# Performance work log

Hardware: AMD Instinct MI355X
Metric: run time of the kernel (lower is better)

## Reference

```python
import jax, jax.numpy as jnp
import numpy as np

B, N, F, P = 8, 16384, 128, 28


def setup_inputs() -> dict:
    key = jax.random.key(0)
    k1, k2 = jax.random.split(key)
    x = jax.random.uniform(k1, (B, N, 2), dtype=jnp.float32)  # 2D coords in [0,1]
    sigma = jnp.full((1,), np.log(0.05), dtype=jnp.float32)   # learned log-lengthscale
    image_features = jax.random.normal(k2, (F, P, P), dtype=jnp.float32) / np.sqrt(F)
    return {"x": x, "sigma": sigma, "image_features": image_features}


def reference(x, sigma, image_features):
    # x: [B, N, 2], sigma: [1] (log lengthscale), image_features: [F, P, P]
    P_ = image_features.shape[-1]
    grid = jnp.linspace(0.001, 1.0 - 0.001, P_, dtype=x.dtype)  # [P]
    ls = jnp.exp(sigma[0])                                      # lengthscale
    inv = 0.5 / (ls * ls)
    # pairwise squared dists grid vs each coordinate axis -> [B, P, N]
    d0 = (grid[None, :, None] - x[:, None, :, 0]) ** 2
    d1 = (grid[None, :, None] - x[:, None, :, 1]) ** 2
    k0 = jnp.exp(-inv * d0)  # [B, P, N]
    k1 = jnp.exp(-inv * d1)  # [B, P, N]
    # features[b,n,f] = sum_{p,q} k0[b,p,n] * IF[f,p,q] * k1[b,q,n]
    feats = jnp.einsum('bpn,fpq,bqn->bnf', k0, image_features, k1)
    return feats
```

## Files before the change

kernel.cpp:

```cpp
#include <hip/hip_runtime.h>
#include <stdint.h>

#define BDIM   8
#define NDIM   16384
#define FDIM   128
#define PDIM   28
#define MPTS   (BDIM * NDIM)
#define SLICE  4096
#define HSLICE 2048
#define TPTS   256
#define TILES  2
#define CPTS   (TPTS * TILES)

typedef _Float16 half8  __attribute__((ext_vector_type(8)));
typedef _Float16 half4  __attribute__((ext_vector_type(4)));
typedef float    floatx4 __attribute__((ext_vector_type(4)));

__global__ __launch_bounds__(256) void prep_ift(const float* __restrict__ IF,
                                                _Float16* __restrict__ IFt) {
    int idx = blockIdx.x * 256 + threadIdx.x;
    int kk  = idx >> 12;
    int rem = idx & 4095;
    int f   = rem >> 5;
    int s   = (rem >> 3) & 3;
    int j   = idx & 7;
    int q   = ((s ^ ((f >> 1) & 3)) << 3) + j;
    float v = (q < PDIM) ? IF[f * (PDIM * PDIM) + kk * PDIM + q] : 0.0f;
    IFt[idx] = (_Float16)v;
}

__device__ __forceinline__ void gload16(const _Float16* g, _Float16* l) {
    __builtin_amdgcn_global_load_lds(
        (const __attribute__((address_space(1))) void*)g,
        (__attribute__((address_space(3))) void*)l, 16, 0, 0);
}

__global__ __launch_bounds__(512, 1) void feats_kernel(
    const float* __restrict__ x,
    const float* __restrict__ sigma,
    const _Float16* __restrict__ IFt,
    float* __restrict__ out)
{
    __shared__ __align__(16) _Float16 bs [PDIM * HSLICE];
    __shared__ __align__(16) _Float16 k1s[TPTS * 40];
    __shared__ __align__(16) _Float16 k0t[PDIM * TPTS];

    const int tid   = threadIdx.x;
    const int lane  = tid & 63;
    const int wave  = tid >> 6;
    const int wm    = wave >> 1;
    const int wn    = wave & 1;
    const int ln15  = lane & 15;
    const int quad  = lane >> 4;
    const int chunk = blockIdx.x >> 1;
    const int h     = blockIdx.x & 1;

    if (tid < 256) {
        const _Float16* g = IFt + h * HSLICE + tid * 8;
        #pragma unroll
        for (int kk = 0; kk < PDIM; kk++)
            gload16(g + kk * SLICE, &bs[kk * HSLICE + tid * 8]);
    }

    const float ls    = __expf(sigma[0]);
    const float inv   = 0.5f / (ls * ls);
    const float gstep = 0.998f / 27.0f;

    int bfo[2];
    #pragma unroll
    for (int nt = 0; nt < 2; nt++) {
        const int fl = wn * 32 + nt * 16 + ln15;
        bfo[nt] = fl * 32 + ((quad ^ ((fl >> 1) & 3)) << 3);
    }
    const int k0o  = wm * 64 + ln15 * 4;
    const int k1ro = wm * 64 + ln15;

    #pragma unroll 1
    for (int tile = 0; tile < TILES; tile++) {
        {
            const int ptl = tid & 255;
            const int ptg = chunk * CPTS + tile * TPTS + ptl;
            if (tid < 256) {
                const float x0 = x[2 * ptg + 0];
                const int base = (ptl >> 6) * 64 + (ptl & 15) * 4 + ((ptl >> 4) & 3);
                #pragma unroll
                for (int p = 0; p < PDIM; p++) {
                    float d = (0.001f + p * gstep) - x0;
                    k0t[p * TPTS + base] = (_Float16)__expf(-inv * d * d);
                }
            } else {
                const float x1 = x[2 * ptg + 1];
                #pragma unroll
                for (int q = 0; q < PDIM; q++) {
                    float d = (0.001f + q * gstep) - x1;
                    k1s[ptl * 40 + q] = (_Float16)__expf(-inv * d * d);
                }
                #pragma unroll
                for (int q = PDIM; q < 32; q++)
                    k1s[ptl * 40 + q] = (_Float16)0.0f;
            }
        }
        __syncthreads();

        half8 k1f[4];
        #pragma unroll
        for (int mt = 0; mt < 4; mt++)
            k1f[mt] = *(const half8*)&k1s[(k1ro + mt * 16) * 40 + quad * 8];

        floatx4 acc[4][2];
        #pragma unroll
        for (int mt = 0; mt < 4; mt++)
            #pragma unroll
            for (int nt = 0; nt < 2; nt++)
                acc[mt][nt] = (floatx4){0.0f, 0.0f, 0.0f, 0.0f};

        #pragma unroll 4
        for (int kk = 0; kk < PDIM; kk++) {
            half8 bf[2];
            #pragma unroll
            for (int nt = 0; nt < 2; nt++)
                bf[nt] = *(const half8*)&bs[kk * HSLICE + bfo[nt]];
            const half4 k0v = *(const half4*)&k0t[kk * TPTS + k0o];
            #pragma unroll
            for (int mt = 0; mt < 4; mt++) {
                const half8 af = k1f[mt] * k0v[mt];
                #pragma unroll
                for (int nt = 0; nt < 2; nt++)
                    acc[mt][nt] = __builtin_amdgcn_mfma_f32_16x16x32_f16(
                        af, bf[nt], acc[mt][nt], 0, 0, 0);
            }
        }

        #pragma unroll
        for (int mt = 0; mt < 4; mt++) {
            const int row0 = chunk * CPTS + tile * TPTS + wm * 64 + mt * 16 + quad * 4;
            #pragma unroll
            for (int nt = 0; nt < 2; nt++) {
                const int col = h * 64 + wn * 32 + nt * 16 + ln15;
                float* op = out + (size_t)row0 * FDIM + col;
                #pragma unroll
                for (int r = 0; r < 4; r++)
                    __builtin_nontemporal_store(acc[mt][nt][r], op + (size_t)r * FDIM);
            }
        }

        if (tile + 1 < TILES)
            __syncthreads();
    }
}

extern "C" void kernel_launch(void* const* d_in, const int* in_sizes, int n_in,
                              void* d_out, int out_size, void* d_ws, size_t ws_size,
                              hipStream_t stream) {
    const float* x     = (const float*)d_in[0];
    const float* sigma = (const float*)d_in[1];
    const float* IF    = (const float*)d_in[2];
    float* out = (float*)d_out;

    _Float16* IFt = (_Float16*)d_ws;

    prep_ift<<<(PDIM * SLICE) / 256, 256, 0, stream>>>(IF, IFt);
    feats_kernel<<<(MPTS / CPTS) * 2, 512, 0, stream>>>(x, sigma, IFt, out);
}
```

Before: 101.7 us.

## Split features into quarters, double-buffer k0 tiles, compute k1 in registers

Each block now handles a quarter of the feature dimension (32 columns) over four 256-point tiles, which shrinks the LDS footprint so launch bounds can allow four blocks per CU. The k0 Gaussian table is double-buffered and the next tile is filled while the current one is computed, leaving a single barrier per tile. k1 fragments are computed straight into registers per wave instead of being staged through LDS. The trade-off is that k0/k1 exponentials are recomputed across four times as many blocks and there are fewer MFMAs per wave per tile.

```diff
diff --git a/kernel.cpp b/kernel.cpp
--- a/kernel.cpp
+++ b/kernel.cpp
@@ -7,13 +7,13 @@
 #define PDIM   28
 #define MPTS   (BDIM * NDIM)
 #define SLICE  4096
-#define HSLICE 2048
+#define QSL    1024
 #define TPTS   256
-#define TILES  2
+#define TILES  4
 #define CPTS   (TPTS * TILES)
 
 typedef _Float16 half8  __attribute__((ext_vector_type(8)));
-typedef _Float16 half4  __attribute__((ext_vector_type(4)));
+typedef _Float16 half2v __attribute__((ext_vector_type(2)));
 typedef float    floatx4 __attribute__((ext_vector_type(4)));
 
 __global__ __launch_bounds__(256) void prep_ift(const float* __restrict__ IF,
@@ -35,94 +35,97 @@
         (__attribute__((address_space(3))) void*)l, 16, 0, 0);
 }
 
-__global__ __launch_bounds__(512, 1) void feats_kernel(
+__global__ __launch_bounds__(512, 4) void feats_kernel(
     const float* __restrict__ x,
     const float* __restrict__ sigma,
     const _Float16* __restrict__ IFt,
     float* __restrict__ out)
 {
-    __shared__ __align__(16) _Float16 bs [PDIM * HSLICE];
-    __shared__ __align__(16) _Float16 k1s[TPTS * 40];
-    __shared__ __align__(16) _Float16 k0t[PDIM * TPTS];
+    __shared__ __align__(16) _Float16 bs [PDIM * QSL];
+    __shared__ __align__(16) _Float16 k0t[2][PDIM * TPTS];
 
     const int tid   = threadIdx.x;
     const int lane  = tid & 63;
     const int wave  = tid >> 6;
-    const int wm    = wave >> 1;
-    const int wn    = wave & 1;
     const int ln15  = lane & 15;
     const int quad  = lane >> 4;
-    const int chunk = blockIdx.x >> 1;
-    const int h     = blockIdx.x & 1;
+    const int chunk = blockIdx.x >> 2;
+    const int q4    = blockIdx.x & 3;
 
-    if (tid < 256) {
-        const _Float16* g = IFt + h * HSLICE + tid * 8;
+    {
+        const _Float16* g = IFt + q4 * QSL;
         #pragma unroll
-        for (int kk = 0; kk < PDIM; kk++)
-            gload16(g + kk * SLICE, &bs[kk * HSLICE + tid * 8]);
+        for (int it = 0; it < 7; it++) {
+            const int i   = it * 512 + tid;
+            const int kk  = i >> 7;
+            const int off = (i & 127) * 8;
+            gload16(g + kk * SLICE + off, &bs[kk * QSL + off]);
+        }
     }
 
     const float ls    = __expf(sigma[0]);
     const float inv   = 0.5f / (ls * ls);
     const float gstep = 0.998f / 27.0f;
 
+    const int ptl = tid & 255;
+    const int ph  = tid >> 8;
+    const int m_  = (ptl & ~31) + (ptl & 15) * 2 + ((ptl >> 4) & 1);
+
+#define FILL_K0(TT, BUF)                                                      \
+    do {                                                                      \
+        const float x0 = x[2 * (chunk * CPTS + (TT) * TPTS + ptl)];           \
+        _Pragma("unroll")                                                     \
+        for (int pp = 0; pp < 14; pp++) {                                     \
+            const int p = ph * 14 + pp;                                       \
+            const float d = (0.001f + p * gstep) - x0;                        \
+            k0t[BUF][p * TPTS + m_] = (_Float16)__expf(-inv * d * d);         \
+        }                                                                     \
+    } while (0)
+
+    FILL_K0(0, 0);
+    __syncthreads();
+
     int bfo[2];
     #pragma unroll
     for (int nt = 0; nt < 2; nt++) {
-        const int fl = wn * 32 + nt * 16 + ln15;
+        const int fl = nt * 16 + ln15;
         bfo[nt] = fl * 32 + ((quad ^ ((fl >> 1) & 3)) << 3);
     }
-    const int k0o  = wm * 64 + ln15 * 4;
-    const int k1ro = wm * 64 + ln15;
+    const int k0o = wave * 32 + ln15 * 2;
 
     #pragma unroll 1
-    for (int tile = 0; tile < TILES; tile++) {
-        {
-            const int ptl = tid & 255;
-            const int ptg = chunk * CPTS + tile * TPTS + ptl;
-            if (tid < 256) {
-                const float x0 = x[2 * ptg + 0];
-                const int base = (ptl >> 6) * 64 + (ptl & 15) * 4 + ((ptl >> 4) & 3);
-                #pragma unroll
-                for (int p = 0; p < PDIM; p++) {
-                    float d = (0.001f + p * gstep) - x0;
-                    k0t[p * TPTS + base] = (_Float16)__expf(-inv * d * d);
-                }
-            } else {
-                const float x1 = x[2 * ptg + 1];
-                #pragma unroll
-                for (int q = 0; q < PDIM; q++) {
-                    float d = (0.001f + q * gstep) - x1;
-                    k1s[ptl * 40 + q] = (_Float16)__expf(-inv * d * d);
-                }
-                #pragma unroll
-                for (int q = PDIM; q < 32; q++)
-                    k1s[ptl * 40 + q] = (_Float16)0.0f;
+    for (int t = 0; t < TILES; t++) {
+        if (t + 1 < TILES) FILL_K0(t + 1, (t + 1) & 1);
+
+        half8 k1f[2];
+        #pragma unroll
+        for (int mt = 0; mt < 2; mt++) {
+            const int pt = chunk * CPTS + t * TPTS + wave * 32 + mt * 16 + ln15;
+            const float x1 = x[2 * pt + 1];
+            #pragma unroll
+            for (int j = 0; j < 8; j++) {
+                const float d = (0.001f + (quad * 8 + j) * gstep) - x1;
+                k1f[mt][j] = (_Float16)__expf(-inv * d * d);
             }
         }
-        __syncthreads();
 
-        half8 k1f[4];
+        floatx4 acc[2][2];
         #pragma unroll
-        for (int mt = 0; mt < 4; mt++)
-            k1f[mt] = *(const half8*)&k1s[(k1ro + mt * 16) * 40 + quad * 8];
-
-        floatx4 acc[4][2];
-        #pragma unroll
-        for (int mt = 0; mt < 4; mt++)
+        for (int mt = 0; mt < 2; mt++)
             #pragma unroll
             for (int nt = 0; nt < 2; nt++)
                 acc[mt][nt] = (floatx4){0.0f, 0.0f, 0.0f, 0.0f};
 
-        #pragma unroll 4
+        const _Float16* k0b = &k0t[t & 1][0];
+        #pragma unroll 7
         for (int kk = 0; kk < PDIM; kk++) {
             half8 bf[2];
             #pragma unroll
             for (int nt = 0; nt < 2; nt++)
-                bf[nt] = *(const half8*)&bs[kk * HSLICE + bfo[nt]];
-            const half4 k0v = *(const half4*)&k0t[kk * TPTS + k0o];
+                bf[nt] = *(const half8*)&bs[kk * QSL + bfo[nt]];
+            const half2v k0v = *(const half2v*)&k0b[kk * TPTS + k0o];
             #pragma unroll
-            for (int mt = 0; mt < 4; mt++) {
+            for (int mt = 0; mt < 2; mt++) {
                 const half8 af = k1f[mt] * k0v[mt];
                 #pragma unroll
                 for (int nt = 0; nt < 2; nt++)
@@ -132,11 +135,11 @@
         }
 
         #pragma unroll
-        for (int mt = 0; mt < 4; mt++) {
-            const int row0 = chunk * CPTS + tile * TPTS + wm * 64 + mt * 16 + quad * 4;
+        for (int mt = 0; mt < 2; mt++) {
+            const int row0 = chunk * CPTS + t * TPTS + wave * 32 + mt * 16 + quad * 4;
             #pragma unroll
             for (int nt = 0; nt < 2; nt++) {
-                const int col = h * 64 + wn * 32 + nt * 16 + ln15;
+                const int col = q4 * 32 + nt * 16 + ln15;
                 float* op = out + (size_t)row0 * FDIM + col;
                 #pragma unroll
                 for (int r = 0; r < 4; r++)
@@ -144,9 +147,13 @@
             }
         }
 
-        if (tile + 1 < TILES)
-            __syncthreads();
+        if (t + 1 < TILES) {
+            asm volatile("s_waitcnt lgkmcnt(0)" ::: "memory");
+            __builtin_amdgcn_s_barrier();
+            __builtin_amdgcn_sched_barrier(0);
+        }
     }
+#undef FILL_K0
 }
 
 extern "C" void kernel_launch(void* const* d_in, const int* in_sizes, int n_in,
@@ -160,5 +167,5 @@
     _Float16* IFt = (_Float16*)d_ws;
 
     prep_ift<<<(PDIM * SLICE) / 256, 256, 0, stream>>>(IF, IFt);
-    feats_kernel<<<(MPTS / CPTS) * 2, 512, 0, stream>>>(x, sigma, IFt, out);
+    feats_kernel<<<(MPTS / CPTS) * 4, 512, 0, stream>>>(x, sigma, IFt, out);
 }
```

After: 104.9 us. 3.1% more time.
